# Kernel tuning notes

Hardware: AMD Instinct MI355X
Metric: run time of the kernel (lower is better)

## Reference

```python
import jax, jax.numpy as jnp
import numpy as np

HIDDEN = 1024
HEADS = 16
HEAD_DIM = HIDDEN // HEADS
SCALE = float(np.sqrt(HEAD_DIM))
B, S = 4, 2048


def setup_inputs() -> dict:
    key = jax.random.key(0)
    ks = jax.random.split(key, 10)
    inp = {
        "query": jax.random.normal(ks[0], (B, S, HIDDEN), dtype=jnp.float32),
        "mask": jax.random.randint(ks[1], (B, S), 0, 2).astype(jnp.bool_),
        "Wq": jax.random.normal(ks[2], (HIDDEN, HIDDEN), dtype=jnp.float32) * 0.02,
        "bq": jax.random.normal(ks[3], (HIDDEN,), dtype=jnp.float32) * 0.02,
        "Wk": jax.random.normal(ks[4], (HIDDEN, HIDDEN), dtype=jnp.float32) * 0.02,
        "bk": jax.random.normal(ks[5], (HIDDEN,), dtype=jnp.float32) * 0.02,
        "Wv": jax.random.normal(ks[6], (HIDDEN, HIDDEN), dtype=jnp.float32) * 0.02,
        "bv": jax.random.normal(ks[7], (HIDDEN,), dtype=jnp.float32) * 0.02,
        "Wo": jax.random.normal(ks[8], (HIDDEN, HIDDEN), dtype=jnp.float32) * 0.02,
        "bo": jax.random.normal(ks[9], (HIDDEN,), dtype=jnp.float32) * 0.02,
    }
    return inp


def reference(query, mask, Wq, bq, Wk, bk, Wv, bv, Wo, bo):
    b, s, _ = query.shape
    # QKV projections (torch Linear: x @ W.T + b)
    q = query @ Wq.T + bq
    k = query @ Wk.T + bk
    v = query @ Wv.T + bv
    # [b, h, s, d]
    q = q.reshape(b, s, HEADS, HEAD_DIM).transpose(0, 2, 1, 3)
    k = k.reshape(b, s, HEADS, HEAD_DIM).transpose(0, 2, 1, 3)
    v = v.reshape(b, s, HEADS, HEAD_DIM).transpose(0, 2, 1, 3)
    # energy[b,h,i,j] = q_i . k_j / scale
    energy = jnp.einsum("bhid,bhjd->bhij", q, k) / SCALE
    m = mask.astype(energy.dtype)
    energy = energy * m[:, None, :, None] * m[:, None, None, :]
    # NOTE: softmax over the QUERY axis (dim=2), not the key axis
    attention = jax.nn.softmax(energy, axis=2)
    x = jnp.einsum("bhij,bhjd->bhid", attention, v)
    x = x.transpose(0, 2, 1, 3).reshape(b, s, HIDDEN)
    out = x @ Wo.T + bo
    return jnp.squeeze(out)
```

## Files before the change

kernel.cpp:

```cpp
#include <hip/hip_runtime.h>

#define SQ   2048
#define HIDN 1024
#define NB   4
#define NH   16
#define HD   64

typedef __attribute__((ext_vector_type(8))) short short8;
typedef __attribute__((ext_vector_type(4))) short short4v;
typedef __attribute__((ext_vector_type(4))) float f32x4;

__device__ __forceinline__ short f2bf(float f) {
  union { float f; unsigned u; } x; x.f = f;
  unsigned r = (x.u + 0x7fffu + ((x.u >> 16) & 1u)) >> 16;
  return (short)r;
}

__device__ __forceinline__ unsigned cvtpk_bf16(float lo, float hi) {
  unsigned u;
  asm("v_cvt_pk_bf16_f32 %0, %1, %2" : "=v"(u) : "v"(lo), "v"(hi));
  return u;
}

__device__ __forceinline__ float exp2_raw(float x) {
  float r;
  asm("v_exp_f32 %0, %1" : "=v"(r) : "v"(x));
  return r;
}

#define MFMA(a, b, c) __builtin_amdgcn_mfma_f32_16x16x32_bf16((a), (b), (c), 0, 0, 0)

__device__ __forceinline__ void gload16(const void* g, void* l) {
  __builtin_amdgcn_global_load_lds(
      (const __attribute__((address_space(1))) unsigned*)g,
      (__attribute__((address_space(3))) unsigned*)l, 16, 0, 0);
}

#define LOG2E 1.44269504f

__global__ __launch_bounds__(256) void k_maskprep(const unsigned* __restrict__ mraw,
                                                  float* __restrict__ m) {
  __shared__ unsigned red[256];
  const int tid = threadIdx.x;
  unsigned w_or = 0;
  for (int i = tid; i < 2048; i += 256) w_or |= mraw[i];
  red[tid] = w_or;
  __syncthreads();
  for (int s = 128; s > 0; s >>= 1) {
    if (tid < s) red[tid] |= red[tid + s];
    __syncthreads();
  }
  const unsigned allw = red[0];
  int mode;
  if ((allw & 0xFFFFFFFEu) == 0) mode = 0;
  else if ((allw & 0xFEFEFEFEu) == 0) mode = 1;
  else mode = 2;
  const unsigned char* mb = (const unsigned char*)mraw;
  const float* mf = (const float*)mraw;
  const int* mi = (const int*)mraw;
  for (int i = tid; i < NB * SQ; i += 256) {
    float v;
    if (mode == 0)      v = mi[i] ? 1.0f : 0.0f;
    else if (mode == 1) v = mb[i] ? 1.0f : 0.0f;
    else                v = (mf[i] != 0.0f) ? 1.0f : 0.0f;
    m[i] = v;
  }
}

__global__ __launch_bounds__(256) void k_cvt(
    const float* __restrict__ query, const float* __restrict__ Wq,
    const float* __restrict__ Wk, const float* __restrict__ Wv,
    short* __restrict__ qbf, short* __restrict__ wbf)
{
  const int yy = blockIdx.y;
  const float* __restrict__ src = (yy == 0) ? query : (yy == 1) ? Wq : (yy == 2) ? Wk : Wv;
  short* __restrict__ dst = (yy == 0) ? qbf : wbf + (yy - 1) * (HIDN * HIDN);
  const int n = (yy == 0) ? (NB * SQ * HIDN) : (HIDN * HIDN);
  const int i = (blockIdx.x * 256 + threadIdx.x) * 4;
  if (i >= n) return;
  const f32x4 v = *(const f32x4*)(src + i);
  short4v s;
#pragma unroll
  for (int e = 0; e < 4; ++e) s[e] = f2bf(v[e]);
  *(short4v*)(dst + i) = s;
}

__global__ __launch_bounds__(256) void k_cvtWo(
    const float* __restrict__ Wo, short* __restrict__ wo)
{
  const int i = (blockIdx.x * 256 + threadIdx.x) * 4;
  if (i >= HIDN * HIDN) return;
  const f32x4 v = *(const f32x4*)(Wo + i);
  short4v s;
#pragma unroll
  for (int e = 0; e < 4; ++e) s[e] = f2bf(v[e]);
  *(short4v*)(wo + i) = s;
}

__global__ __launch_bounds__(256) void k_proj_qkv2(
    const short* __restrict__ qbf, const short* __restrict__ wbf,
    const float* __restrict__ bq, const float* __restrict__ bkb,
    const float* __restrict__ bv, const float* __restrict__ mfl,
    short* __restrict__ qh, short* __restrict__ kh, short* __restrict__ vT)
{
  __shared__ short a_s[128 * 64];
  __shared__ short b_s[128 * 64];
  const int nt = blockIdx.x, mt = blockIdx.y;
  const int tid = threadIdx.x;
  const int w = tid >> 6, lane = tid & 63;
  const int wr = w >> 1, wc = w & 1;
  const int lg = lane >> 4, lr = lane & 15;

  const int z = nt >> 3;
  const float* __restrict__ bias = (z == 0) ? bq : (z == 1) ? bkb : bv;

  int srow[4], scs[4], sbase[4];
#pragma unroll
  for (int p = 0; p < 4; ++p) {
    const int id = p * 256 + tid;
    const int r = id >> 3, c = id & 7;
    srow[p] = r;
    scs[p] = c ^ (r & 7);
    sbase[p] = (p * 256 + w * 64) * 8;
  }

  f32x4 acc[4][4] = {};

  for (int k0 = 0; k0 < HIDN; k0 += 64) {
#pragma unroll
    for (int p = 0; p < 4; ++p) {
      const short* ga = qbf + (size_t)(mt * 128 + srow[p]) * HIDN + k0 + scs[p] * 8;
      const short* gb = wbf + (size_t)(nt * 128 + srow[p]) * HIDN + k0 + scs[p] * 8;
      gload16(ga, a_s + sbase[p]);
      gload16(gb, b_s + sbase[p]);
    }
    __syncthreads();
#pragma unroll
    for (int kk = 0; kk < 2; ++kk) {
      short8 af[4], bfv[4];
#pragma unroll
      for (int mi = 0; mi < 4; ++mi) {
        const int r = wr * 64 + mi * 16 + lr;
        const int phys = (kk * 4 + lg) ^ (r & 7);
        af[mi] = *(const short8*)((const char*)a_s + r * 128 + phys * 16);
      }
#pragma unroll
      for (int ni = 0; ni < 4; ++ni) {
        const int r = wc * 64 + ni * 16 + lr;
        const int phys = (kk * 4 + lg) ^ (r & 7);
        bfv[ni] = *(const short8*)((const char*)b_s + r * 128 + phys * 16);
      }
#pragma unroll
      for (int mi = 0; mi < 4; ++mi)
#pragma unroll
        for (int ni = 0; ni < 4; ++ni)
          acc[mi][ni] = MFMA(af[mi], bfv[ni], acc[mi][ni]);
    }
    __syncthreads();
  }

#pragma unroll
  for (int mi = 0; mi < 4; ++mi)
#pragma unroll
    for (int ni = 0; ni < 4; ++ni)
#pragma unroll
      for (int r = 0; r < 4; ++r) {
        const int row = mt * 128 + wr * 64 + mi * 16 + lg * 4 + r;
        const int colz = (nt & 7) * 128 + wc * 64 + ni * 16 + lr;
        const float v = acc[mi][ni][r] + bias[colz];
        const int bi = row >> 11, s = row & (SQ - 1);
        const int h = colz >> 6, d = colz & (HD - 1);
        if (z == 0) {
          qh[(((bi * NH + h) * SQ + s) * HD) + d] = f2bf(v * (0.125f * LOG2E) * mfl[row]);
        } else if (z == 1) {
          kh[(((bi * NH + h) * SQ + s) * HD) + d] = f2bf(v * mfl[row]);
        } else {
          vT[(((bi * NH + h) * HD + d) * SQ) + s] = f2bf(v);
        }
      }
}

__global__ __launch_bounds__(256) void k_sumexp_m(
    const short* __restrict__ qh, const short* __restrict__ kh,
    float* __restrict__ rcpL)
{
  __shared__ short q_s[2][64][72];
  const int bh = blockIdx.y;
  const int jt = blockIdx.x;
  const int tid = threadIdx.x, w = tid >> 6, lane = tid & 63;
  const int lg = lane >> 4, lr = lane & 15;

  const int base = bh * SQ * HD;
  const int jbase = jt * 256 + w * 64;

  short8 bk[4][2];
#pragma unroll
  for (int jf = 0; jf < 4; ++jf) {
    const int j = jbase + jf * 16 + lr;
    bk[jf][0] = *(const short8*)(kh + base + j * HD + lg * 8);
    bk[jf][1] = *(const short8*)(kh + base + j * HD + 32 + lg * 8);
  }

  const int srow = tid >> 3, scc = (tid & 7) * 8;
  {
    const short8 s0 = *(const short8*)(qh + base + srow * HD + scc);
    const short8 s1 = *(const short8*)(qh + base + (32 + srow) * HD + scc);
    *(short8*)&q_s[0][srow][scc] = s0;
    *(short8*)&q_s[0][32 + srow][scc] = s1;
  }
  __syncthreads();

  f32x4 Lacc[4] = {};
  for (int t = 0; t < 32; ++t) {
    const int cur = t & 1;
    short8 n0, n1;
    if (t < 31) {
      const int ibn = (t + 1) * 64;
      n0 = *(const short8*)(qh + base + (ibn + srow) * HD + scc);
      n1 = *(const short8*)(qh + base + (ibn + 32 + srow) * HD + scc);
    }
#pragma unroll
    for (int s = 0; s < 4; ++s) {
      const short8 a0 = *(const short8*)&q_s[cur][s * 16 + lr][lg * 8];
      const short8 a1 = *(const short8*)&q_s[cur][s * 16 + lr][32 + lg * 8];
#pragma unroll
      for (int jf = 0; jf < 4; ++jf) {
        f32x4 e = {};
        e = MFMA(a0, bk[jf][0], e);
        e = MFMA(a1, bk[jf][1], e);
#pragma unroll
        for (int r = 0; r < 4; ++r)
          Lacc[jf][r] += exp2_raw(e[r]);
      }
    }
    if (t < 31) {
      __syncthreads();
      *(short8*)&q_s[cur ^ 1][srow][scc] = n0;
      *(short8*)&q_s[cur ^ 1][32 + srow][scc] = n1;
      __syncthreads();
    }
  }

#pragma unroll
  for (int jf = 0; jf < 4; ++jf) {
    float L = Lacc[jf][0] + Lacc[jf][1] + Lacc[jf][2] + Lacc[jf][3];
    L += __shfl_xor(L, 16, 64);
    L += __shfl_xor(L, 32, 64);
    if (lg == 0) rcpL[bh * SQ + jbase + jf * 16 + lr] = 1.0f / L;
  }
}

__global__ __launch_bounds__(256) void k_vscale(
    short* __restrict__ vT, const float* __restrict__ rcpL)
{
  const int idx = blockIdx.x * 256 + threadIdx.x;
  const int basee = idx * 8;
  const int bh = basee >> 17;
  const int s0 = basee & (SQ - 1);
  short8 v = *(const short8*)( (const short*)vT + basee );
  const float* rl = rcpL + bh * SQ + s0;
  float f[8];
#pragma unroll
  for (int e = 0; e < 8; ++e) {
    union { unsigned u; float x; } c;
    c.u = ((unsigned)(unsigned short)v[e]) << 16;
    f[e] = c.x * rl[e];
  }
  union { unsigned u[4]; short8 s8; } o;
#pragma unroll
  for (int e = 0; e < 4; ++e) o.u[e] = cvtpk_bf16(f[2 * e], f[2 * e + 1]);
  *(short8*)( (short*)vT + basee ) = o.s8;
}

__global__ __launch_bounds__(256) void k_attnv(
    const short* __restrict__ qh, const short* __restrict__ kh,
    const short* __restrict__ vT,
    short* __restrict__ xo)
{
  __shared__ __attribute__((aligned(16))) short p_s[4][4][16][40];
  const int bh = blockIdx.y, b = bh >> 4, h = bh & (NH - 1);
  const int it = blockIdx.x;
  const int tid = threadIdx.x, w = tid >> 6, lane = tid & 63;
  const int lg = lane >> 4, lr = lane & 15;

  const int base = bh * SQ * HD;
  const int i0 = it * 256 + w * 64;

  short8 aq[4][2];
#pragma unroll
  for (int fi = 0; fi < 4; ++fi) {
    aq[fi][0] = *(const short8*)(qh + base + (i0 + fi * 16 + lr) * HD + lg * 8);
    aq[fi][1] = *(const short8*)(qh + base + (i0 + fi * 16 + lr) * HD + 32 + lg * 8);
  }

  f32x4 accx[4][4] = {};
  for (int jb = 0; jb < SQ; jb += 32) {
    short8 bk[2][2];
#pragma unroll
    for (int jj = 0; jj < 2; ++jj) {
      const int j = jb + jj * 16 + lr;
      bk[jj][0] = *(const short8*)(kh + base + j * HD + lg * 8);
      bk[jj][1] = *(const short8*)(kh + base + j * HD + 32 + lg * 8);
    }
    short8 bv[4];
#pragma unroll
    for (int nd = 0; nd < 4; ++nd)
      bv[nd] = *(const short8*)(vT + base + (nd * 16 + lr) * SQ + jb + lg * 8);

#pragma unroll
    for (int fi = 0; fi < 4; ++fi) {
      f32x4 e0 = {}, e1 = {};
      e0 = MFMA(bk[0][0], aq[fi][0], e0);
      e0 = MFMA(bk[0][1], aq[fi][1], e0);
      e1 = MFMA(bk[1][0], aq[fi][0], e1);
      e1 = MFMA(bk[1][1], aq[fi][1], e1);
      const unsigned u00 = cvtpk_bf16(exp2_raw(e0[0]), exp2_raw(e0[1]));
      const unsigned u01 = cvtpk_bf16(exp2_raw(e0[2]), exp2_raw(e0[3]));
      const unsigned u10 = cvtpk_bf16(exp2_raw(e1[0]), exp2_raw(e1[1]));
      const unsigned u11 = cvtpk_bf16(exp2_raw(e1[2]), exp2_raw(e1[3]));
      uint2 w0; w0.x = u00; w0.y = u01;
      uint2 w1; w1.x = u10; w1.y = u11;
      *(uint2*)&p_s[w][fi][lr][lg * 4] = w0;
      *(uint2*)&p_s[w][fi][lr][16 + lg * 4] = w1;
    }
#pragma unroll
    for (int fi = 0; fi < 4; ++fi) {
      const short8 pa = *(const short8*)&p_s[w][fi][lr][lg * 8];
#pragma unroll
      for (int nd = 0; nd < 4; ++nd)
        accx[fi][nd] = MFMA(pa, bv[nd], accx[fi][nd]);
    }
  }

#pragma unroll
  for (int fi = 0; fi < 4; ++fi)
#pragma unroll
    for (int nd = 0; nd < 4; ++nd)
#pragma unroll
      for (int r = 0; r < 4; ++r) {
        const int i = i0 + fi * 16 + lg * 4 + r, d = nd * 16 + lr;
        xo[(b * SQ + i) * HIDN + h * HD + d] = f2bf(accx[fi][nd][r]);
      }
}

__global__ __launch_bounds__(256) void k_proj_out2(
    const short* __restrict__ xb, const short* __restrict__ wo,
    const float* __restrict__ bo, float* __restrict__ out)
{
  __shared__ short a_s[128 * 64];
  __shared__ short b_s[128 * 64];
  const int nt = blockIdx.x, mt = blockIdx.y;
  const int tid = threadIdx.x;
  const int w = tid >> 6, lane = tid & 63;
  const int wr = w >> 1, wc = w & 1;
  const int lg = lane >> 4, lr = lane & 15;

  int srow[4], scs[4], sbase[4];
#pragma unroll
  for (int p = 0; p < 4; ++p) {
    const int id = p * 256 + tid;
    const int r = id >> 3, c = id & 7;
    srow[p] = r;
    scs[p] = c ^ (r & 7);
    sbase[p] = (p * 256 + w * 64) * 8;
  }

  f32x4 acc[4][4] = {};

  for (int k0 = 0; k0 < HIDN; k0 += 64) {
#pragma unroll
    for (int p = 0; p < 4; ++p) {
      const short* ga = xb + (size_t)(mt * 128 + srow[p]) * HIDN + k0 + scs[p] * 8;
      const short* gb = wo + (size_t)(nt * 128 + srow[p]) * HIDN + k0 + scs[p] * 8;
      gload16(ga, a_s + sbase[p]);
      gload16(gb, b_s + sbase[p]);
    }
    __syncthreads();
#pragma unroll
    for (int kk = 0; kk < 2; ++kk) {
      short8 af[4], bfv[4];
#pragma unroll
      for (int mi = 0; mi < 4; ++mi) {
        const int r = wr * 64 + mi * 16 + lr;
        const int phys = (kk * 4 + lg) ^ (r & 7);
        af[mi] = *(const short8*)((const char*)a_s + r * 128 + phys * 16);
      }
#pragma unroll
      for (int ni = 0; ni < 4; ++ni) {
        const int r = wc * 64 + ni * 16 + lr;
        const int phys = (kk * 4 + lg) ^ (r & 7);
        bfv[ni] = *(const short8*)((const char*)b_s + r * 128 + phys * 16);
      }
#pragma unroll
      for (int mi = 0; mi < 4; ++mi)
#pragma unroll
        for (int ni = 0; ni < 4; ++ni)
          acc[mi][ni] = MFMA(af[mi], bfv[ni], acc[mi][ni]);
    }
    __syncthreads();
  }

#pragma unroll
  for (int mi = 0; mi < 4; ++mi)
#pragma unroll
    for (int ni = 0; ni < 4; ++ni)
#pragma unroll
      for (int r = 0; r < 4; ++r) {
        const int row = mt * 128 + wr * 64 + mi * 16 + lg * 4 + r;
        const int col = nt * 128 + wc * 64 + ni * 16 + lr;
        out[row * HIDN + col] = acc[mi][ni][r] + bo[col];
      }
}

extern "C" void kernel_launch(void* const* d_in, const int* in_sizes, int n_in,
                              void* d_out, int out_size, void* d_ws, size_t ws_size,
                              hipStream_t stream) {
  const float* query = (const float*)d_in[0];
  const unsigned* mraw = (const unsigned*)d_in[1];
  const float* Wq = (const float*)d_in[2];
  const float* bq = (const float*)d_in[3];
  const float* Wk = (const float*)d_in[4];
  const float* bk = (const float*)d_in[5];
  const float* Wv = (const float*)d_in[6];
  const float* bv = (const float*)d_in[7];
  const float* Wo = (const float*)d_in[8];
  const float* bo = (const float*)d_in[9];

  short* qh  = (short*)d_ws;
  short* kh  = qh + (NB * NH * SQ * HD);
  short* vT  = kh + (NB * NH * SQ * HD);
  short* xb  = vT + (NB * NH * SQ * HD);
  float* rcpL = (float*)(xb + (NB * SQ * HIDN));
  float* mfl = rcpL + (NB * NH * SQ);

  short* qbf = (short*)d_out;
  short* wbf = qbf + (NB * SQ * HIDN);
  short* wo  = qh;

  k_maskprep<<<dim3(1), dim3(256), 0, stream>>>(mraw, mfl);
  k_cvt<<<dim3((NB * SQ * HIDN) / 1024, 4), dim3(256), 0, stream>>>(
      query, Wq, Wk, Wv, qbf, wbf);
  k_proj_qkv2<<<dim3(24, 64), dim3(256), 0, stream>>>(
      qbf, wbf, bq, bk, bv, mfl, qh, kh, vT);
  k_sumexp_m<<<dim3(SQ / 256, NB * NH), dim3(256), 0, stream>>>(qh, kh, rcpL);
  k_vscale<<<dim3((NB * NH * HD * SQ) / (256 * 8)), dim3(256), 0, stream>>>(vT, rcpL);
  k_attnv<<<dim3(SQ / 256, NB * NH), dim3(256), 0, stream>>>(qh, kh, vT, xb);
  k_cvtWo<<<dim3((HIDN * HIDN) / 1024), dim3(256), 0, stream>>>(Wo, wo);
  k_proj_out2<<<dim3(HIDN / 128, (NB * SQ) / 128), dim3(256), 0, stream>>>(
      xb, wo, bo, (float*)d_out);
}
```

Baseline: 339.6 us.

## Stage K and V tiles in shared memory with swizzled layout in attnv kernel

The attention-times-V kernel now loads 64-row K and V tiles cooperatively into shared memory using direct global-to-LDS loads with an XOR swizzle. Each wave then reads its MFMA operands from LDS instead of issuing redundant per-wave global loads, and the key step grows from 32 to 64. This cuts global and L2 traffic, since four waves previously each fetched the same K/V, but adds two block barriers per iteration with no double buffering, so load latency is no longer hidden.

```diff
diff --git a/kernel.cpp b/kernel.cpp
--- a/kernel.cpp
+++ b/kernel.cpp
@@ -277,6 +277,8 @@
     const short* __restrict__ vT,
     short* __restrict__ xo)
 {
+  __shared__ short k_s[64 * 64];
+  __shared__ short v_s[64 * 64];
   __shared__ __attribute__((aligned(16))) short p_s[4][4][16][40];
   const int bh = blockIdx.y, b = bh >> 4, h = bh & (NH - 1);
   const int it = blockIdx.x;
@@ -293,43 +295,71 @@
     aq[fi][1] = *(const short8*)(qh + base + (i0 + fi * 16 + lr) * HD + 32 + lg * 8);
   }
 
+  int strow[2], stphys[2], stbase[2];
+#pragma unroll
+  for (int p = 0; p < 2; ++p) {
+    const int id = p * 256 + tid;
+    const int r = id >> 3, c = id & 7;
+    strow[p] = r;
+    stphys[p] = c ^ (r & 7);
+    stbase[p] = (p * 256 + w * 64) * 8;
+  }
+
   f32x4 accx[4][4] = {};
-  for (int jb = 0; jb < SQ; jb += 32) {
-    short8 bk[2][2];
-#pragma unroll
-    for (int jj = 0; jj < 2; ++jj) {
-      const int j = jb + jj * 16 + lr;
-      bk[jj][0] = *(const short8*)(kh + base + j * HD + lg * 8);
-      bk[jj][1] = *(const short8*)(kh + base + j * HD + 32 + lg * 8);
-    }
-    short8 bv[4];
-#pragma unroll
-    for (int nd = 0; nd < 4; ++nd)
-      bv[nd] = *(const short8*)(vT + base + (nd * 16 + lr) * SQ + jb + lg * 8);
-
-#pragma unroll
-    for (int fi = 0; fi < 4; ++fi) {
-      f32x4 e0 = {}, e1 = {};
-      e0 = MFMA(bk[0][0], aq[fi][0], e0);
-      e0 = MFMA(bk[0][1], aq[fi][1], e0);
-      e1 = MFMA(bk[1][0], aq[fi][0], e1);
-      e1 = MFMA(bk[1][1], aq[fi][1], e1);
-      const unsigned u00 = cvtpk_bf16(exp2_raw(e0[0]), exp2_raw(e0[1]));
-      const unsigned u01 = cvtpk_bf16(exp2_raw(e0[2]), exp2_raw(e0[3]));
-      const unsigned u10 = cvtpk_bf16(exp2_raw(e1[0]), exp2_raw(e1[1]));
-      const unsigned u11 = cvtpk_bf16(exp2_raw(e1[2]), exp2_raw(e1[3]));
-      uint2 w0; w0.x = u00; w0.y = u01;
-      uint2 w1; w1.x = u10; w1.y = u11;
-      *(uint2*)&p_s[w][fi][lr][lg * 4] = w0;
-      *(uint2*)&p_s[w][fi][lr][16 + lg * 4] = w1;
-    }
-#pragma unroll
-    for (int fi = 0; fi < 4; ++fi) {
-      const short8 pa = *(const short8*)&p_s[w][fi][lr][lg * 8];
-#pragma unroll
-      for (int nd = 0; nd < 4; ++nd)
-        accx[fi][nd] = MFMA(pa, bv[nd], accx[fi][nd]);
-    }
+  for (int jb = 0; jb < SQ; jb += 64) {
+#pragma unroll
+    for (int p = 0; p < 2; ++p) {
+      gload16(kh + base + (size_t)(jb + strow[p]) * HD + stphys[p] * 8,
+              k_s + stbase[p]);
+      gload16(vT + base + (size_t)strow[p] * SQ + jb + stphys[p] * 8,
+              v_s + stbase[p]);
+    }
+    __syncthreads();
+
+#pragma unroll
+    for (int sub = 0; sub < 2; ++sub) {
+      short8 bk[2][2];
+#pragma unroll
+      for (int jj = 0; jj < 2; ++jj) {
+        const int rr = sub * 32 + jj * 16 + lr;
+        const int ph0 = lg ^ (rr & 7);
+        const int ph1 = (4 + lg) ^ (rr & 7);
+        bk[jj][0] = *(const short8*)(k_s + rr * 64 + ph0 * 8);
+        bk[jj][1] = *(const short8*)(k_s + rr * 64 + ph1 * 8);
+      }
+      short8 bv[4];
+#pragma unroll
+      for (int nd = 0; nd < 4; ++nd) {
+        const int rv = nd * 16 + lr;
+        const int ph = (sub * 4 + lg) ^ (rv & 7);
+        bv[nd] = *(const short8*)(v_s + rv * 64 + ph * 8);
+      }
+
+#pragma unroll
+      for (int fi = 0; fi < 4; ++fi) {
+        f32x4 e0 = {}, e1 = {};
+        e0 = MFMA(bk[0][0], aq[fi][0], e0);
+        e0 = MFMA(bk[0][1], aq[fi][1], e0);
+        e1 = MFMA(bk[1][0], aq[fi][0], e1);
+        e1 = MFMA(bk[1][1], aq[fi][1], e1);
+        const unsigned u00 = cvtpk_bf16(exp2_raw(e0[0]), exp2_raw(e0[1]));
+        const unsigned u01 = cvtpk_bf16(exp2_raw(e0[2]), exp2_raw(e0[3]));
+        const unsigned u10 = cvtpk_bf16(exp2_raw(e1[0]), exp2_raw(e1[1]));
+        const unsigned u11 = cvtpk_bf16(exp2_raw(e1[2]), exp2_raw(e1[3]));
+        uint2 w0; w0.x = u00; w0.y = u01;
+        uint2 w1; w1.x = u10; w1.y = u11;
+        *(uint2*)&p_s[w][fi][lr][lg * 4] = w0;
+        *(uint2*)&p_s[w][fi][lr][16 + lg * 4] = w1;
+      }
+#pragma unroll
+      for (int fi = 0; fi < 4; ++fi) {
+        const short8 pa = *(const short8*)&p_s[w][fi][lr][lg * 8];
+#pragma unroll
+        for (int nd = 0; nd < 4; ++nd)
+          accx[fi][nd] = MFMA(pa, bv[nd], accx[fi][nd]);
+      }
+    }
+    __syncthreads();
   }
 
 #pragma unroll
```

Result: faster. 296.4 us (-12.7%).
